# Performance work log

Hardware: AMD Instinct MI355X
Metric: run time of the kernel (lower is better)

Reference implementation:

```python
import jax, jax.numpy as jnp
import numpy as np

B, S, E, H = 2, 2048, 1024, 16
D = E // H

def setup_inputs() -> dict:
    key = jax.random.key(0)
    ks = jax.random.split(key, 11)
    sc = 0.02
    inp = {
        'queries': jax.random.normal(ks[0], (B, S, E), jnp.float32),
        'keys':    jax.random.normal(ks[1], (B, S, E), jnp.float32),
        'values':  jax.random.normal(ks[2], (B, S, E), jnp.float32),
        'Wq': jax.random.normal(ks[3], (E, E), jnp.float32) * sc,
        'bq': jnp.zeros((E,), jnp.float32),
        'Wk': jax.random.normal(ks[4], (E, E), jnp.float32) * sc,
        'bk': jnp.zeros((E,), jnp.float32),
        'Wv': jax.random.normal(ks[5], (E, E), jnp.float32) * sc,
        'bv': jnp.zeros((E,), jnp.float32),
        'Wo': jax.random.normal(ks[6], (E, E), jnp.float32) * sc,
        'bo': jnp.zeros((E,), jnp.float32),
        'indicator': 0,
    }
    return inp

def reference(queries, keys, values, Wq, bq, Wk, bk, Wv, bv, Wo, bo, indicator):
    # torch Linear: y = x @ W.T + b
    q = queries @ Wq.T + bq
    k = keys    @ Wk.T + bk
    v = values  @ Wv.T + bv
    # [B,S,E] -> [B,H,S,D]
    q = q.reshape(B, S, H, D).transpose(0, 2, 1, 3)
    k = k.reshape(B, S, H, D).transpose(0, 2, 1, 3)
    v = v.reshape(B, S, H, D).transpose(0, 2, 1, 3)
    scores = jnp.einsum('bhqd,bhkd->bhqk', q, k) / jnp.sqrt(jnp.float32(D))
    w = jax.nn.sigmoid(scores)
    if indicator != 0:
        w = 1.0 - w
    attn = jax.nn.softmax(w, axis=-1)  # dropout_prob=0 -> identity
    out = jnp.einsum('bhqk,bhkd->bhqd', attn, v)
    out = out.transpose(0, 2, 1, 3).reshape(B, S, E)
    return out @ Wo.T + bo
```

## Files before the change

### kernel.cpp

```cpp
#include <hip/hip_runtime.h>
#include <stdint.h>

#define Bb 2
#define Ss 2048
#define Ee 1024
#define Hh 16
#define Dd 64

typedef __bf16 bf16;
typedef __attribute__((ext_vector_type(8))) __bf16 bf16x8;
typedef __attribute__((ext_vector_type(4))) __bf16 bf16x4;
typedef __attribute__((ext_vector_type(4))) float f32x4;

#define MB (1u << 20)
#define OFF_XQ 0u
#define OFF_XK (8u * MB)
#define OFF_XV (16u * MB)
#define OFF_WQ (24u * MB)
#define OFF_WK (26u * MB)
#define OFF_WV (28u * MB)
#define OFF_WO (30u * MB)
#define OFF_Q  (32u * MB)
#define OFF_K  (40u * MB)
#define OFF_VT (48u * MB)
#define OFF_AO (56u * MB)

__device__ __forceinline__ void gll16(const void* g, void* lds) {
  __builtin_amdgcn_global_load_lds(
      (const __attribute__((address_space(1))) void*)g,
      (__attribute__((address_space(3))) void*)lds, 16, 0, 0);
}

__device__ __forceinline__ unsigned pkbf(float lo, float hi) {
  unsigned r;
  asm("v_cvt_pk_bf16_f32 %0, %1, %2" : "=v"(r) : "v"(lo), "v"(hi));
  return r;
}
#define PL32SWAP(a, b) asm("v_permlane32_swap_b32 %0, %1" : "+v"(a), "+v"(b))
#define PL16SWAP(a, b) asm("v_permlane16_swap_b32 %0, %1" : "+v"(a), "+v"(b))

__global__ __launch_bounds__(256) void convert_kernel(
    const float* __restrict__ q, const float* __restrict__ k, const float* __restrict__ v,
    const float* __restrict__ wq, const float* __restrict__ wk, const float* __restrict__ wv,
    const float* __restrict__ wo, const int* __restrict__ ind, char* __restrict__ ws)
{
  const unsigned base = blockIdx.x * 256u + threadIdx.x;
#pragma unroll
  for (unsigned it = 0; it < 4; ++it) {
    const unsigned i = base + it * 1048576u;
    const float* src;
    bf16* dst;
    float scale = 1.0f;
    if (i < 3145728u) {
      const unsigned a = i >> 20, j = i & 1048575u;
      src = (a == 0 ? q : a == 1 ? k : v) + (size_t)j * 4;
      dst = (bf16*)(ws + (size_t)a * (8u * MB)) + (size_t)j * 4;
    } else {
      const unsigned i2 = i - 3145728u;
      const unsigned a = i2 >> 18, j = i2 & 262143u;
      src = (a == 0 ? wq : a == 1 ? wk : a == 2 ? wv : wo) + (size_t)j * 4;
      dst = (bf16*)(ws + OFF_WQ + (size_t)a * (2u * MB)) + (size_t)j * 4;
      if (a == 0) {
        const float c1v = (*ind != 0) ? 1.442695041f : -1.442695041f;
        scale = 0.125f * c1v;
      }
    }
    const float4 f = *(const float4*)src;
    bf16x4 o;
    o[0] = (bf16)(f.x * scale);
    o[1] = (bf16)(f.y * scale);
    o[2] = (bf16)(f.z * scale);
    o[3] = (bf16)(f.w * scale);
    *(bf16x4*)dst = o;
  }
}

template <bool TR>
__device__ __forceinline__ void gemm128_body(
    const bf16* __restrict__ A, const bf16* __restrict__ W,
    char* smem, int m0, int n0, int t, f32x4 (&acc)[4][4])
{
  char* As = smem;
  char* Bs = smem + 16384;
  const int lane = t & 63;
  const int wid = t >> 6;
  const int wm = (wid >> 1) << 6;
  const int wn = (wid & 1) << 6;
  for (int kt = 0; kt < 1024; kt += 64) {
    __syncthreads();
#pragma unroll
    for (int i = 0; i < 4; ++i) {
      const int L = i * 4096 + t * 16;
      const int r = L >> 7;
      const int c = ((L >> 4) & 7) ^ (r & 7);
      gll16(A + (size_t)(m0 + r) * 1024 + kt + c * 8, As + i * 4096 + wid * 1024);
      gll16(W + (size_t)(n0 + r) * 1024 + kt + c * 8, Bs + i * 4096 + wid * 1024);
    }
    __syncthreads();
#pragma unroll
    for (int ks = 0; ks < 2; ++ks) {
      bf16x8 af[4], bff[4];
#pragma unroll
      for (int mi = 0; mi < 4; ++mi) {
        const int r = wm + mi * 16 + (lane & 15);
        const int c = (ks * 4 + (lane >> 4)) ^ (r & 7);
        af[mi] = *(const bf16x8*)(As + r * 128 + c * 16);
      }
#pragma unroll
      for (int ni = 0; ni < 4; ++ni) {
        const int r = wn + ni * 16 + (lane & 15);
        const int c = (ks * 4 + (lane >> 4)) ^ (r & 7);
        bff[ni] = *(const bf16x8*)(Bs + r * 128 + c * 16);
      }
      __builtin_amdgcn_s_setprio(1);
#pragma unroll
      for (int mi = 0; mi < 4; ++mi)
#pragma unroll
        for (int ni = 0; ni < 4; ++ni) {
          if (TR)
            acc[mi][ni] = __builtin_amdgcn_mfma_f32_16x16x32_bf16(bff[ni], af[mi], acc[mi][ni], 0, 0, 0);
          else
            acc[mi][ni] = __builtin_amdgcn_mfma_f32_16x16x32_bf16(af[mi], bff[ni], acc[mi][ni], 0, 0, 0);
        }
      __builtin_amdgcn_s_setprio(0);
    }
  }
}

__global__ __launch_bounds__(256) void proj_gemm(
    char* __restrict__ ws, const float* __restrict__ bq,
    const float* __restrict__ bk, const float* __restrict__ bv,
    const int* __restrict__ ind)
{
  __shared__ __align__(16) char smem[32768];
  const int zi = blockIdx.z;
  const bf16* A = (const bf16*)(ws + (zi == 0 ? OFF_XQ : zi == 1 ? OFF_XK : OFF_XV));
  const bf16* W = (const bf16*)(ws + (zi == 0 ? OFF_WQ : zi == 1 ? OFF_WK : OFF_WV));
  const float* bias = zi == 0 ? bq : zi == 1 ? bk : bv;
  bf16* outp = (bf16*)(ws + (zi == 0 ? OFF_Q : zi == 1 ? OFF_K : OFF_VT));
  const float c1v = (*ind != 0) ? 1.442695041f : -1.442695041f;
  const float bscale = (zi == 0) ? 0.125f * c1v : 1.0f;
  const int t = threadIdx.x;
  const int wgid = blockIdx.x + blockIdx.y * 8;
  const int nw = (wgid & 7) * 32 + (wgid >> 3);
  const int m0 = (nw >> 3) * 128, n0 = (nw & 7) * 128;
  const int lane = t & 63, wid = t >> 6;
  const int wm = (wid >> 1) << 6, wn = (wid & 1) << 6;
  const int l15 = lane & 15, g = lane >> 4;
  f32x4 acc[4][4] = {};
  if (zi == 2) {
    gemm128_body<false>(A, W, smem, m0, n0, t, acc);
#pragma unroll
    for (int ni = 0; ni < 4; ++ni) {
      const int col = n0 + wn + ni * 16 + l15;
      const float bvv = bias[col];
      const int h = col >> 6, d = col & 63;
#pragma unroll
      for (int mi = 0; mi < 4; ++mi) {
        const int row0 = m0 + wm + mi * 16 + g * 4;
        const int b = row0 >> 11, s = row0 & 2047;
        bf16x4 o;
#pragma unroll
        for (int r2 = 0; r2 < 4; ++r2) o[r2] = (bf16)(acc[mi][ni][r2] + bvv);
        *(bf16x4*)&outp[((size_t)((b * Hh + h) * Dd + d) * Ss) + s] = o;
      }
    }
  } else {
    gemm128_body<true>(A, W, smem, m0, n0, t, acc);
#pragma unroll
    for (int mi = 0; mi < 4; ++mi) {
      const int row = m0 + wm + mi * 16 + l15;
      const int b = row >> 11, s = row & 2047;
#pragma unroll
      for (int ni = 0; ni < 4; ++ni) {
        const int col0 = n0 + wn + ni * 16 + g * 4;
        const int h = col0 >> 6, d0 = col0 & 63;
        const float4 b4 = *(const float4*)&bias[col0];
        bf16x4 o;
        o[0] = (bf16)(acc[mi][ni][0] + b4.x * bscale);
        o[1] = (bf16)(acc[mi][ni][1] + b4.y * bscale);
        o[2] = (bf16)(acc[mi][ni][2] + b4.z * bscale);
        o[3] = (bf16)(acc[mi][ni][3] + b4.w * bscale);
        *(bf16x4*)&outp[((size_t)((b * Hh + h) * Ss + s) * Dd) + d0] = o;
      }
    }
  }
}

__global__ __launch_bounds__(256, 2) void attn_kernel(char* __restrict__ ws)
{
  __shared__ __align__(16) char smem[65536];
  char* Os = smem;
  const int t = threadIdx.x, lane = t & 63, wid = t >> 6;
  const int g = lane >> 4, l15 = lane & 15;
  const int lin = blockIdx.x;
  const int j = lin >> 3;
  const int bh = ((lin & 7) << 2) + (j & 3);
  const int q0 = (j >> 2) << 7;
  const bf16* Qg  = (const bf16*)(ws + OFF_Q)  + (size_t)bh * Ss * Dd;
  const bf16* Kg  = (const bf16*)(ws + OFF_K)  + (size_t)bh * Ss * Dd;
  const bf16* Vtg = (const bf16*)(ws + OFF_VT) + (size_t)bh * Ss * Dd;
  bf16* AO = (bf16*)(ws + OFF_AO);

  bf16x8 qf[2][2];
#pragma unroll
  for (int qh = 0; qh < 2; ++qh)
#pragma unroll
    for (int ks = 0; ks < 2; ++ks)
      qf[qh][ks] = *(const bf16x8*)(Qg + (size_t)(q0 + wid * 32 + qh * 16 + l15) * Dd + ks * 32 + g * 8);

  f32x4 acc_o[2][4] = {};
  f32x4 acc_sum[2] = {};
  union { unsigned u[4]; bf16x8 v; } ones_;
#pragma unroll
  for (int jj = 0; jj < 4; ++jj) ones_.u[jj] = 0x3F803F80u;

#define STAGE_KV(kt_, buf_)                                                         \
  {                                                                                  \
    char* Kb = (buf_);                                                               \
    char* Vb = (buf_) + 16384;                                                       \
    _Pragma("unroll")                                                                \
    for (int i = 0; i < 4; ++i) {                                                    \
      const int L = i * 4096 + t * 16;                                               \
      const int rk = L >> 7;                                                         \
      const int ck = ((L >> 4) & 7) ^ (rk & 7);                                      \
      gll16(Kg + (size_t)((kt_) + rk) * Dd + ck * 8, Kb + i * 4096 + wid * 1024);    \
      const int rv = L >> 8;                                                         \
      const int cv = ((L >> 4) & 15) ^ (rv & 15);                                    \
      gll16(Vtg + (size_t)rv * Ss + (kt_) + cv * 8, Vb + i * 4096 + wid * 1024);     \
    }                                                                                \
  }

  STAGE_KV(0, smem);
  __syncthreads();

  for (int ti = 0; ti < 16; ++ti) {
    char* cur = smem + (ti & 1) * 32768;
    char* nxt = smem + ((ti & 1) ^ 1) * 32768;
    if (ti < 15) STAGE_KV((ti + 1) * 128, nxt);
    char* Ks = cur;
    char* Vts = cur + 16384;

    f32x4 st[2][8];
#pragma unroll
    for (int qh = 0; qh < 2; ++qh)
#pragma unroll
      for (int ni = 0; ni < 8; ++ni)
        st[qh][ni] = (f32x4){-0.52876637f, -0.52876637f, -0.52876637f, -0.52876637f};
    __builtin_amdgcn_s_setprio(1);
#pragma unroll
    for (int ks = 0; ks < 2; ++ks) {
#pragma unroll
      for (int ni = 0; ni < 8; ++ni) {
        const int r = ni * 16 + l15;
        const int c = (ks * 4 + g) ^ (r & 7);
        const bf16x8 kf = *(const bf16x8*)(Ks + r * 128 + c * 16);
        st[0][ni] = __builtin_amdgcn_mfma_f32_16x16x32_bf16(kf, qf[0][ks], st[0][ni], 0, 0, 0);
        st[1][ni] = __builtin_amdgcn_mfma_f32_16x16x32_bf16(kf, qf[1][ks], st[1][ni], 0, 0, 0);
      }
    }
    __builtin_amdgcn_s_setprio(0);

#pragma unroll
    for (int kb = 0; kb < 4; ++kb) {
      union { unsigned u[4]; bf16x8 v; } pb[2];
#pragma unroll
      for (int qh = 0; qh < 2; ++qh) {
        float p[2][4];
#pragma unroll
        for (int e = 0; e < 2; ++e)
#pragma unroll
          for (int r2 = 0; r2 < 4; ++r2) {
            const float ex = __builtin_amdgcn_exp2f(st[qh][2 * kb + e][r2]);
            const float tt = __builtin_amdgcn_rcpf(0.69314718f + ex);
            p[e][r2] = __builtin_amdgcn_exp2f(tt);
          }
        unsigned E0 = pkbf(p[0][0], p[0][1]);
        unsigned E1 = pkbf(p[0][2], p[0][3]);
        unsigned O0 = pkbf(p[1][0], p[1][1]);
        unsigned O1 = pkbf(p[1][2], p[1][3]);
        PL32SWAP(E0, O0);
        PL16SWAP(E0, O0);
        PL32SWAP(E1, O1);
        PL16SWAP(E1, O1);
        pb[qh].u[0] = E0; pb[qh].u[1] = E1; pb[qh].u[2] = O0; pb[qh].u[3] = O1;
      }
      __builtin_amdgcn_s_setprio(1);
#pragma unroll
      for (int dblk = 0; dblk < 4; ++dblk) {
        const int r = dblk * 16 + l15;
        const int c = (kb * 4 + g) ^ (r & 15);
        const bf16x8 vf = *(const bf16x8*)(Vts + r * 256 + c * 16);
        acc_o[0][dblk] = __builtin_amdgcn_mfma_f32_16x16x32_bf16(vf, pb[0].v, acc_o[0][dblk], 0, 0, 0);
        acc_o[1][dblk] = __builtin_amdgcn_mfma_f32_16x16x32_bf16(vf, pb[1].v, acc_o[1][dblk], 0, 0, 0);
      }
      acc_sum[0] = __builtin_amdgcn_mfma_f32_16x16x32_bf16(ones_.v, pb[0].v, acc_sum[0], 0, 0, 0);
      acc_sum[1] = __builtin_amdgcn_mfma_f32_16x16x32_bf16(ones_.v, pb[1].v, acc_sum[1], 0, 0, 0);
      __builtin_amdgcn_s_setprio(0);
    }
    __syncthreads();
  }
#undef STAGE_KV

  const float rinv[2] = {__builtin_amdgcn_rcpf(acc_sum[0][0]),
                         __builtin_amdgcn_rcpf(acc_sum[1][0])};

#pragma unroll
  for (int qh = 0; qh < 2; ++qh) {
    const int row = wid * 32 + qh * 16 + l15;
#pragma unroll
    for (int dblk = 0; dblk < 4; ++dblk) {
      const unsigned w0 = pkbf(acc_o[qh][dblk][0] * rinv[qh], acc_o[qh][dblk][1] * rinv[qh]);
      const unsigned w1 = pkbf(acc_o[qh][dblk][2] * rinv[qh], acc_o[qh][dblk][3] * rinv[qh]);
      const int cc = dblk * 2 + (g >> 1);
      char* a = Os + row * 128 + (cc ^ (row & 7)) * 16 + (g & 1) * 8;
      *(uint2*)a = make_uint2(w0, w1);
    }
  }
  __syncthreads();
  const int b = bh >> 4, h = bh & 15;
#pragma unroll
  for (int i = 0; i < 4; ++i) {
    const int L = i * 4096 + t * 16;
    const int r = L >> 7;
    const int cc = (L >> 4) & 7;
    const uint4 w = *(const uint4*)(Os + r * 128 + (cc ^ (r & 7)) * 16);
    *(uint4*)&AO[((size_t)(b * Ss + q0 + r) << 10) + h * 64 + cc * 8] = w;
  }
}

__global__ __launch_bounds__(256) void out_gemm(char* __restrict__ ws,
                                                const float* __restrict__ bo,
                                                float* __restrict__ outp)
{
  __shared__ __align__(16) char smem[24576];
  char* As = smem;
  char* Bs = smem + 16384;
  const bf16* A = (const bf16*)(ws + OFF_AO);
  const bf16* W = (const bf16*)(ws + OFF_WO);
  const int t = threadIdx.x, lane = t & 63, wid = t >> 6;
  const int l15 = lane & 15, g = lane >> 4;
  const int wgid = blockIdx.x + blockIdx.y * 16;
  const int nw = (wgid & 7) * 64 + (wgid >> 3);
  const int m0 = (nw >> 4) * 128, n0 = (nw & 15) * 64;
  const int wm = (wid >> 1) << 6;
  const int wn = (wid & 1) << 5;
  f32x4 acc[4][2] = {};
  for (int kt = 0; kt < 1024; kt += 64) {
    __syncthreads();
#pragma unroll
    for (int i = 0; i < 4; ++i) {
      const int L = i * 4096 + t * 16;
      const int r = L >> 7;
      const int c = ((L >> 4) & 7) ^ (r & 7);
      gll16(A + (size_t)(m0 + r) * 1024 + kt + c * 8, As + i * 4096 + wid * 1024);
    }
#pragma unroll
    for (int i = 0; i < 2; ++i) {
      const int L = i * 4096 + t * 16;
      const int r = L >> 7;
      const int c = ((L >> 4) & 7) ^ (r & 7);
      gll16(W + (size_t)(n0 + r) * 1024 + kt + c * 8, Bs + i * 4096 + wid * 1024);
    }
    __syncthreads();
#pragma unroll
    for (int ks = 0; ks < 2; ++ks) {
      bf16x8 af[4], bff[2];
#pragma unroll
      for (int mi = 0; mi < 4; ++mi) {
        const int r = wm + mi * 16 + l15;
        const int c = (ks * 4 + g) ^ (r & 7);
        af[mi] = *(const bf16x8*)(As + r * 128 + c * 16);
      }
#pragma unroll
      for (int ni = 0; ni < 2; ++ni) {
        const int r = wn + ni * 16 + l15;
        const int c = (ks * 4 + g) ^ (r & 7);
        bff[ni] = *(const bf16x8*)(Bs + r * 128 + c * 16);
      }
      __builtin_amdgcn_s_setprio(1);
#pragma unroll
      for (int mi = 0; mi < 4; ++mi)
#pragma unroll
        for (int ni = 0; ni < 2; ++ni)
          acc[mi][ni] = __builtin_amdgcn_mfma_f32_16x16x32_bf16(bff[ni], af[mi], acc[mi][ni], 0, 0, 0);
      __builtin_amdgcn_s_setprio(0);
    }
  }
#pragma unroll
  for (int mi = 0; mi < 4; ++mi) {
    const int row = m0 + wm + mi * 16 + l15;
#pragma unroll
    for (int ni = 0; ni < 2; ++ni) {
      const int col0 = n0 + wn + ni * 16 + g * 4;
      const float4 b4 = *(const float4*)&bo[col0];
      float4 o;
      o.x = acc[mi][ni][0] + b4.x;
      o.y = acc[mi][ni][1] + b4.y;
      o.z = acc[mi][ni][2] + b4.z;
      o.w = acc[mi][ni][3] + b4.w;
      *(float4*)&outp[(size_t)row * Ee + col0] = o;
    }
  }
}

extern "C" void kernel_launch(void* const* d_in, const int* in_sizes, int n_in,
                              void* d_out, int out_size, void* d_ws, size_t ws_size,
                              hipStream_t stream) {
  (void)in_sizes; (void)n_in; (void)out_size; (void)ws_size;
  const float* queries = (const float*)d_in[0];
  const float* keys    = (const float*)d_in[1];
  const float* values  = (const float*)d_in[2];
  const float* Wq = (const float*)d_in[3];
  const float* bq = (const float*)d_in[4];
  const float* Wk = (const float*)d_in[5];
  const float* bk = (const float*)d_in[6];
  const float* Wv = (const float*)d_in[7];
  const float* bv = (const float*)d_in[8];
  const float* Wo = (const float*)d_in[9];
  const float* bo = (const float*)d_in[10];
  const int* indicator = (const int*)d_in[11];
  char* ws = (char*)d_ws;
  float* outp = (float*)d_out;

  convert_kernel<<<4096, 256, 0, stream>>>(queries, keys, values, Wq, Wk, Wv, Wo, indicator, ws);
  proj_gemm<<<dim3(8, 32, 3), 256, 0, stream>>>(ws, bq, bk, bv, indicator);
  attn_kernel<<<512, 256, 0, stream>>>(ws);
  out_gemm<<<dim3(16, 32), 256, 0, stream>>>(ws, bo, outp);
}
```

Before: 233.0 us.

## Double-buffer GEMM LDS tiles with explicit vmcnt waits and raw barriers

The projection and output GEMMs now use two LDS buffers, so the next K-tile's global-to-LDS loads are issued before the current tile is computed. Each wait is a partial vmcnt wait that leaves only the newest loads outstanding. The attention loop's __syncthreads calls are replaced with the same explicit vmcnt/lgkmcnt waits plus s_barrier and sched_barrier, which keeps the prefetch in flight across the barrier. The goal is to hide global load latency behind MFMA work, at the cost of doubled LDS per block, which may reduce occupancy.

```diff
diff --git a/kernel.cpp b/kernel.cpp
--- a/kernel.cpp
+++ b/kernel.cpp
@@ -76,40 +76,53 @@
 }
 
 template <bool TR>
-__device__ __forceinline__ void gemm128_body(
+__device__ __forceinline__ void gemm128_db(
     const bf16* __restrict__ A, const bf16* __restrict__ W,
     char* smem, int m0, int n0, int t, f32x4 (&acc)[4][4])
 {
-  char* As = smem;
-  char* Bs = smem + 16384;
   const int lane = t & 63;
   const int wid = t >> 6;
   const int wm = (wid >> 1) << 6;
   const int wn = (wid & 1) << 6;
-  for (int kt = 0; kt < 1024; kt += 64) {
-    __syncthreads();
-#pragma unroll
-    for (int i = 0; i < 4; ++i) {
-      const int L = i * 4096 + t * 16;
-      const int r = L >> 7;
-      const int c = ((L >> 4) & 7) ^ (r & 7);
-      gll16(A + (size_t)(m0 + r) * 1024 + kt + c * 8, As + i * 4096 + wid * 1024);
-      gll16(W + (size_t)(n0 + r) * 1024 + kt + c * 8, Bs + i * 4096 + wid * 1024);
-    }
-    __syncthreads();
+  const int l15 = lane & 15, g = lane >> 4;
+#define PSTAGE(kt_, b_)                                                               \
+  {                                                                                    \
+    char* Ab = smem + (b_) * 32768;                                                    \
+    char* Bb2 = Ab + 16384;                                                            \
+    _Pragma("unroll")                                                                  \
+    for (int i = 0; i < 4; ++i) {                                                      \
+      const int L = i * 4096 + t * 16;                                                 \
+      const int r = L >> 7;                                                            \
+      const int c = ((L >> 4) & 7) ^ (r & 7);                                          \
+      gll16(A + (size_t)(m0 + r) * 1024 + (kt_) + c * 8, Ab + i * 4096 + wid * 1024);  \
+      gll16(W + (size_t)(n0 + r) * 1024 + (kt_) + c * 8, Bb2 + i * 4096 + wid * 1024); \
+    }                                                                                  \
+  }
+  PSTAGE(0, 0);
+  for (int step = 0; step < 16; ++step) {
+    if (step < 15) {
+      PSTAGE((step + 1) * 64, (step + 1) & 1);
+      asm volatile("s_waitcnt vmcnt(8)" ::: "memory");
+    } else {
+      asm volatile("s_waitcnt vmcnt(0)" ::: "memory");
+    }
+    __builtin_amdgcn_s_barrier();
+    __builtin_amdgcn_sched_barrier(0);
+    char* As = smem + (step & 1) * 32768;
+    char* Bs = As + 16384;
 #pragma unroll
     for (int ks = 0; ks < 2; ++ks) {
       bf16x8 af[4], bff[4];
 #pragma unroll
       for (int mi = 0; mi < 4; ++mi) {
-        const int r = wm + mi * 16 + (lane & 15);
-        const int c = (ks * 4 + (lane >> 4)) ^ (r & 7);
+        const int r = wm + mi * 16 + l15;
+        const int c = (ks * 4 + g) ^ (r & 7);
         af[mi] = *(const bf16x8*)(As + r * 128 + c * 16);
       }
 #pragma unroll
       for (int ni = 0; ni < 4; ++ni) {
-        const int r = wn + ni * 16 + (lane & 15);
-        const int c = (ks * 4 + (lane >> 4)) ^ (r & 7);
+        const int r = wn + ni * 16 + l15;
+        const int c = (ks * 4 + g) ^ (r & 7);
         bff[ni] = *(const bf16x8*)(Bs + r * 128 + c * 16);
       }
       __builtin_amdgcn_s_setprio(1);
@@ -124,7 +137,11 @@
         }
       __builtin_amdgcn_s_setprio(0);
     }
-  }
+    asm volatile("s_waitcnt lgkmcnt(0)" ::: "memory");
+    __builtin_amdgcn_s_barrier();
+    __builtin_amdgcn_sched_barrier(0);
+  }
+#undef PSTAGE
 }
 
 __global__ __launch_bounds__(256) void proj_gemm(
@@ -132,7 +149,7 @@
     const float* __restrict__ bk, const float* __restrict__ bv,
     const int* __restrict__ ind)
 {
-  __shared__ __align__(16) char smem[32768];
+  __shared__ __align__(16) char smem[65536];
   const int zi = blockIdx.z;
   const bf16* A = (const bf16*)(ws + (zi == 0 ? OFF_XQ : zi == 1 ? OFF_XK : OFF_XV));
   const bf16* W = (const bf16*)(ws + (zi == 0 ? OFF_WQ : zi == 1 ? OFF_WK : OFF_WV));
@@ -149,7 +166,7 @@
   const int l15 = lane & 15, g = lane >> 4;
   f32x4 acc[4][4] = {};
   if (zi == 2) {
-    gemm128_body<false>(A, W, smem, m0, n0, t, acc);
+    gemm128_db<false>(A, W, smem, m0, n0, t, acc);
 #pragma unroll
     for (int ni = 0; ni < 4; ++ni) {
       const int col = n0 + wn + ni * 16 + l15;
@@ -166,7 +183,7 @@
       }
     }
   } else {
-    gemm128_body<true>(A, W, smem, m0, n0, t, acc);
+    gemm128_db<true>(A, W, smem, m0, n0, t, acc);
 #pragma unroll
     for (int mi = 0; mi < 4; ++mi) {
       const int row = m0 + wm + mi * 16 + l15;
@@ -232,12 +249,18 @@
   }
 
   STAGE_KV(0, smem);
-  __syncthreads();
 
   for (int ti = 0; ti < 16; ++ti) {
     char* cur = smem + (ti & 1) * 32768;
     char* nxt = smem + ((ti & 1) ^ 1) * 32768;
-    if (ti < 15) STAGE_KV((ti + 1) * 128, nxt);
+    if (ti < 15) {
+      STAGE_KV((ti + 1) * 128, nxt);
+      asm volatile("s_waitcnt vmcnt(8)" ::: "memory");
+    } else {
+      asm volatile("s_waitcnt vmcnt(0)" ::: "memory");
+    }
+    __builtin_amdgcn_s_barrier();
+    __builtin_amdgcn_sched_barrier(0);
     char* Ks = cur;
     char* Vts = cur + 16384;
 
@@ -298,7 +321,9 @@
       acc_sum[1] = __builtin_amdgcn_mfma_f32_16x16x32_bf16(ones_.v, pb[1].v, acc_sum[1], 0, 0, 0);
       __builtin_amdgcn_s_setprio(0);
     }
-    __syncthreads();
+    asm volatile("s_waitcnt lgkmcnt(0)" ::: "memory");
+    __builtin_amdgcn_s_barrier();
+    __builtin_amdgcn_sched_barrier(0);
   }
 #undef STAGE_KV
 
@@ -333,9 +358,7 @@
                                                 const float* __restrict__ bo,
                                                 float* __restrict__ outp)
 {
-  __shared__ __align__(16) char smem[24576];
-  char* As = smem;
-  char* Bs = smem + 16384;
+  __shared__ __align__(16) char smem[49152];
   const bf16* A = (const bf16*)(ws + OFF_AO);
   const bf16* W = (const bf16*)(ws + OFF_WO);
   const int t = threadIdx.x, lane = t & 63, wid = t >> 6;
@@ -346,23 +369,37 @@
   const int wm = (wid >> 1) << 6;
   const int wn = (wid & 1) << 5;
   f32x4 acc[4][2] = {};
-  for (int kt = 0; kt < 1024; kt += 64) {
-    __syncthreads();
-#pragma unroll
-    for (int i = 0; i < 4; ++i) {
-      const int L = i * 4096 + t * 16;
-      const int r = L >> 7;
-      const int c = ((L >> 4) & 7) ^ (r & 7);
-      gll16(A + (size_t)(m0 + r) * 1024 + kt + c * 8, As + i * 4096 + wid * 1024);
-    }
-#pragma unroll
-    for (int i = 0; i < 2; ++i) {
-      const int L = i * 4096 + t * 16;
-      const int r = L >> 7;
-      const int c = ((L >> 4) & 7) ^ (r & 7);
-      gll16(W + (size_t)(n0 + r) * 1024 + kt + c * 8, Bs + i * 4096 + wid * 1024);
-    }
-    __syncthreads();
+#define OSTAGE(kt_, b_)                                                               \
+  {                                                                                    \
+    char* Ab = smem + (b_) * 24576;                                                    \
+    char* Bb2 = Ab + 16384;                                                            \
+    _Pragma("unroll")                                                                  \
+    for (int i = 0; i < 4; ++i) {                                                      \
+      const int L = i * 4096 + t * 16;                                                 \
+      const int r = L >> 7;                                                            \
+      const int c = ((L >> 4) & 7) ^ (r & 7);                                          \
+      gll16(A + (size_t)(m0 + r) * 1024 + (kt_) + c * 8, Ab + i * 4096 + wid * 1024);  \
+    }                                                                                  \
+    _Pragma("unroll")                                                                  \
+    for (int i = 0; i < 2; ++i) {                                                      \
+      const int L = i * 4096 + t * 16;                                                 \
+      const int r = L >> 7;                                                            \
+      const int c = ((L >> 4) & 7) ^ (r & 7);                                          \
+      gll16(W + (size_t)(n0 + r) * 1024 + (kt_) + c * 8, Bb2 + i * 4096 + wid * 1024); \
+    }                                                                                  \
+  }
+  OSTAGE(0, 0);
+  for (int step = 0; step < 16; ++step) {
+    if (step < 15) {
+      OSTAGE((step + 1) * 64, (step + 1) & 1);
+      asm volatile("s_waitcnt vmcnt(6)" ::: "memory");
+    } else {
+      asm volatile("s_waitcnt vmcnt(0)" ::: "memory");
+    }
+    __builtin_amdgcn_s_barrier();
+    __builtin_amdgcn_sched_barrier(0);
+    char* As = smem + (step & 1) * 24576;
+    char* Bs = As + 16384;
 #pragma unroll
     for (int ks = 0; ks < 2; ++ks) {
       bf16x8 af[4], bff[2];
@@ -386,7 +423,11 @@
           acc[mi][ni] = __builtin_amdgcn_mfma_f32_16x16x32_bf16(bff[ni], af[mi], acc[mi][ni], 0, 0, 0);
       __builtin_amdgcn_s_setprio(0);
     }
-  }
+    asm volatile("s_waitcnt lgkmcnt(0)" ::: "memory");
+    __builtin_amdgcn_s_barrier();
+    __builtin_amdgcn_sched_barrier(0);
+  }
+#undef OSTAGE
 #pragma unroll
   for (int mi = 0; mi < 4; ++mi) {
     const int row = m0 + wm + mi * 16 + l15;
```

Result: faster. 227.6 us (-2.3%).
